# Performance work log

Measured on AMD Instinct MI355X. Metric: run time of the kernel, lower is better.

The kernel has to match this reference:

```python
import jax, jax.numpy as jnp
import numpy as np

N_FEATURES = 64
KERNEL = 3
PAD = KERNEL // 2


def setup_inputs() -> dict:
    key = jax.random.key(0)
    ks = jax.random.split(key, 6)
    B, C, D, H, W = 2, N_FEATURES, 64, 64, 64
    Q = jax.random.normal(ks[0], (B, C, D, H, W), dtype=jnp.float32)
    K = jax.random.normal(ks[1], (B, C, D, H, W), dtype=jnp.float32)
    V = jax.random.normal(ks[2], (B, C, D, H, W), dtype=jnp.float32)
    # learned params: positional embedding (torch.randn init) and 1x1x1 conv
    pos_emb = jax.random.normal(ks[3], (C, KERNEL, KERNEL, KERNEL), dtype=jnp.float32)
    fan_in = C  # 1x1x1 conv fan-in
    bound = 1.0 / np.sqrt(fan_in)
    W_out = jax.random.uniform(ks[4], (C, C), minval=-bound, maxval=bound, dtype=jnp.float32)
    b_out = jax.random.uniform(ks[5], (C,), minval=-bound, maxval=bound, dtype=jnp.float32)
    return {"Q": Q, "K": K, "V": V, "pos_emb": pos_emb, "W_out": W_out, "b_out": b_out}


def reference(Q, K, V, pos_emb, W_out, b_out):
    B, C, D, H, W = Q.shape
    scale = 1.0 / np.sqrt(C).astype(np.float32)
    pad = ((0, 0), (0, 0), (PAD, PAD), (PAD, PAD), (PAD, PAD))
    Kp = jnp.pad(K, pad)
    Vp = jnp.pad(V, pad)
    # scores over the 27 kernel offsets (fixed small loop; data dims vectorized)
    scores = []
    for i in range(KERNEL):
        for j in range(KERNEL):
            for k in range(KERNEL):
                Ks = Kp[:, :, i:i + D, j:j + H, k:k + W]  # (B,C,D,H,W)
                pe = pos_emb[:, i, j, k][None, :, None, None, None]
                scores.append(jnp.sum(Q * (Ks + pe), axis=1) * scale)  # (B,D,H,W)
    attn = jax.nn.softmax(jnp.stack(scores, axis=1), axis=1)  # (B,27,D,H,W)
    x = jnp.zeros_like(Q)
    ijk = 0
    for i in range(KERNEL):
        for j in range(KERNEL):
            for k in range(KERNEL):
                Vs = Vp[:, :, i:i + D, j:j + H, k:k + W]
                x = x + attn[:, ijk][:, None] * Vs
                ijk += 1
    # 1x1x1 conv projection
    out = jnp.einsum('oc,bcdhw->bodhw', W_out, x) + b_out[None, :, None, None, None]
    return out
```

## Files before the change

kernel.cpp:

```cpp
#include <hip/hip_runtime.h>
#include <math.h>

#define CH 64
#define S 64
#define S2 (64 * 64)
#define S3 (64 * 64 * 64)

__device__ float WT_buf[CH * CH];

__global__ __launch_bounds__(256) void wtrans(const float* __restrict__ W) {
  int i = blockIdx.x * 256 + threadIdx.x;
  int o = i >> 6, c = i & 63;
  WT_buf[c * CH + o] = W[o * CH + c];
}

__device__ __forceinline__ unsigned short f2bf(float f) {
  unsigned int u = __float_as_uint(f);
  return (unsigned short)((u + 0x7FFFu + ((u >> 16) & 1u)) >> 16);
}
__device__ __forceinline__ float bf2f(unsigned short s) {
  return __uint_as_float(((unsigned int)s) << 16);
}

__global__ __launch_bounds__(256) void attn_fused(const float* __restrict__ Q,
                                                  const float* __restrict__ K,
                                                  const float* __restrict__ V,
                                                  const float* __restrict__ pe,
                                                  const float* __restrict__ bias,
                                                  float* __restrict__ out) {
  __shared__ unsigned short xs[4][CH][64];
  int tid = threadIdx.x;
  int lane = tid & 63;
  int wv = tid >> 6;

  int raw = blockIdx.x;
  int sw = (raw & 7) * 256 + (raw >> 3);
  int b = sw >> 10;
  int r = sw & 1023;
  int d = r >> 4;
  int hu = __builtin_amdgcn_readfirstlane((r & 15) * 4 + wv);

  size_t bbase = (size_t)b << 24;
  const float* Qb = Q + bbase;
  const float* Kb = K + bbase;
  const float* Vb = V + bbase;
  float* outb = out + bbase;

  float lmL = (lane == 0) ? 0.f : 1.f;
  float lmR = (lane == 63) ? 0.f : 1.f;

  const float* krow[9];
  const float* vrow[9];
  float okf[9];
#pragma unroll
  for (int dz = 0; dz < 3; ++dz)
#pragma unroll
    for (int dy = 0; dy < 3; ++dy) {
      int rr = dz * 3 + dy;
      int zz = d + dz - 1, yy = hu + dy - 1;
      bool ok = ((unsigned)zz < 64u) & ((unsigned)yy < 64u);
      int zc = zz < 0 ? 0 : (zz > 63 ? 63 : zz);
      int yc = yy < 0 ? 0 : (yy > 63 ? 63 : yy);
      krow[rr] = Kb + zc * S2 + yc * S;
      vrow[rr] = Vb + zc * S2 + yc * S;
      okf[rr] = ok ? 1.f : 0.f;
    }
  int pos = d * S2 + hu * S + lane;

  float spe[27];
  float sC[9], sXR[9], sXL[9];
#pragma unroll
  for (int t = 0; t < 27; ++t) spe[t] = 0.f;
#pragma unroll
  for (int rr = 0; rr < 9; ++rr) { sC[rr] = 0.f; sXR[rr] = 0.f; sXL[rr] = 0.f; }

#pragma unroll 4
  for (int c = 0; c < CH; ++c) {
    int coff = c * S3;
    float q = Qb[coff + pos];
    float rv[9];
#pragma unroll
    for (int rr = 0; rr < 9; ++rr) rv[rr] = krow[rr][coff + lane];
    float qR = __shfl_down(q, 1);
    float qL = __shfl_up(q, 1);
#pragma unroll
    for (int rr = 0; rr < 9; ++rr) {
      sC[rr]  = fmaf(q,  rv[rr], sC[rr]);
      sXR[rr] = fmaf(qR, rv[rr], sXR[rr]);
      sXL[rr] = fmaf(qL, rv[rr], sXL[rr]);
    }
    const float* pec = pe + c * 27;
#pragma unroll
    for (int t = 0; t < 27; ++t) spe[t] = fmaf(q, pec[t], spe[t]);
  }

  float s[27];
#pragma unroll
  for (int rr = 0; rr < 9; ++rr) {
    float lt = __shfl_up(sXR[rr], 1);
    float rt = __shfl_down(sXL[rr], 1);
    s[rr * 3]     = fmaf(lt * lmL, okf[rr], spe[rr * 3]);
    s[rr * 3 + 1] = fmaf(sC[rr],   okf[rr], spe[rr * 3 + 1]);
    s[rr * 3 + 2] = fmaf(rt * lmR, okf[rr], spe[rr * 3 + 2]);
  }

  const float SC = 0.125f * 1.44269504088896f;
#pragma unroll
  for (int t = 0; t < 27; ++t) s[t] *= SC;
  float m = s[0];
#pragma unroll
  for (int t = 1; t < 27; ++t) m = fmaxf(m, s[t]);
  float sum = 0.f;
#pragma unroll
  for (int t = 0; t < 27; ++t) {
    s[t] = exp2f(s[t] - m);
    sum += s[t];
  }
  float inv = 1.f / sum;

  float wC[9], sLs[9], sRs[9];
#pragma unroll
  for (int rr = 0; rr < 9; ++rr) {
    float f = inv * okf[rr];
    float wL = s[rr * 3] * f;
    wC[rr]   = s[rr * 3 + 1] * f;
    float wR = s[rr * 3 + 2] * f;
    sLs[rr] = __shfl_down(wL, 1);
    sRs[rr] = __shfl_up(wR, 1);
  }

#pragma unroll 2
  for (int c = 0; c < CH; ++c) {
    int coff = c * S3;
    float rv[9];
#pragma unroll
    for (int rr = 0; rr < 9; ++rr) rv[rr] = vrow[rr][coff + lane];
    float own = 0.f, cR = 0.f, cL = 0.f;
#pragma unroll
    for (int rr = 0; rr < 9; ++rr) {
      own = fmaf(wC[rr], rv[rr], own);
      cR  = fmaf(sLs[rr], rv[rr], cR);
      cL  = fmaf(sRs[rr], rv[rr], cL);
    }
    float x_c = own + __shfl_up(cR, 1) * lmL + __shfl_down(cL, 1) * lmR;
    xs[wv][c][lane] = f2bf(x_c);
  }

#pragma unroll 1
  for (int ot = 0; ot < 4; ++ot) {
    float acc[16];
#pragma unroll
    for (int j = 0; j < 16; ++j) acc[j] = 0.f;
#pragma unroll 4
    for (int c = 0; c < CH; ++c) {
      float xc = bf2f(xs[wv][c][lane]);
      const float* wr = WT_buf + c * CH + ot * 16;
#pragma unroll
      for (int j = 0; j < 16; ++j) acc[j] = fmaf(wr[j], xc, acc[j]);
    }
#pragma unroll
    for (int j = 0; j < 16; ++j)
      outb[(ot * 16 + j) * S3 + pos] = acc[j] + bias[ot * 16 + j];
  }
}

extern "C" void kernel_launch(void* const* d_in, const int* in_sizes, int n_in,
                              void* d_out, int out_size, void* d_ws, size_t ws_size,
                              hipStream_t stream) {
  const float* Q = (const float*)d_in[0];
  const float* K = (const float*)d_in[1];
  const float* V = (const float*)d_in[2];
  const float* pe = (const float*)d_in[3];
  const float* W = (const float*)d_in[4];
  const float* bias = (const float*)d_in[5];
  float* out = (float*)d_out;

  wtrans<<<16, 256, 0, stream>>>(W);
  attn_fused<<<2048, 256, 0, stream>>>(Q, K, V, pe, bias, out);
}
```

Before: 234.7 us.

## Compute 1x1x1 output projection with bf16 MFMA instead of scalar FMAs

The 64x64 output projection now runs on the matrix cores via mfma_f32_16x16x32_bf16, with weights pre-converted to bf16 in a prep kernel and loaded as A fragments. The per-wave x tile in shared memory is transposed to [position][channel] with padding, and pairs of channels are packed per store so B fragments can be read as 8-element vectors. This removes a large scalar FMA loop and the scalar LDS reads, at the cost of bf16 weights (lower precision) and narrower output stores of 16 contiguous positions per row.

```diff
diff --git a/kernel.cpp b/kernel.cpp
--- a/kernel.cpp
+++ b/kernel.cpp
@@ -6,20 +6,19 @@
 #define S2 (64 * 64)
 #define S3 (64 * 64 * 64)
 
-__device__ float WT_buf[CH * CH];
-
-__global__ __launch_bounds__(256) void wtrans(const float* __restrict__ W) {
-  int i = blockIdx.x * 256 + threadIdx.x;
-  int o = i >> 6, c = i & 63;
-  WT_buf[c * CH + o] = W[o * CH + c];
-}
+typedef short short8_t __attribute__((ext_vector_type(8)));
+typedef float float4_t __attribute__((ext_vector_type(4)));
+
+__device__ __align__(16) unsigned short WB_buf[CH * CH];
 
 __device__ __forceinline__ unsigned short f2bf(float f) {
   unsigned int u = __float_as_uint(f);
   return (unsigned short)((u + 0x7FFFu + ((u >> 16) & 1u)) >> 16);
 }
-__device__ __forceinline__ float bf2f(unsigned short s) {
-  return __uint_as_float(((unsigned int)s) << 16);
+
+__global__ __launch_bounds__(256) void wprep(const float* __restrict__ W) {
+  int i = blockIdx.x * 256 + threadIdx.x;
+  WB_buf[i] = f2bf(W[i]);
 }
 
 __global__ __launch_bounds__(256) void attn_fused(const float* __restrict__ Q,
@@ -28,7 +27,7 @@
                                                   const float* __restrict__ pe,
                                                   const float* __restrict__ bias,
                                                   float* __restrict__ out) {
-  __shared__ unsigned short xs[4][CH][64];
+  __shared__ unsigned short xs[4][CH][68];
   int tid = threadIdx.x;
   int lane = tid & 63;
   int wv = tid >> 6;
@@ -65,7 +64,8 @@
       vrow[rr] = Vb + zc * S2 + yc * S;
       okf[rr] = ok ? 1.f : 0.f;
     }
-  int pos = d * S2 + hu * S + lane;
+  int upos = d * S2 + hu * S;
+  int pos = upos + lane;
 
   float spe[27];
   float sC[9], sXR[9], sXL[9];
@@ -130,37 +130,60 @@
   }
 
 #pragma unroll 2
-  for (int c = 0; c < CH; ++c) {
-    int coff = c * S3;
-    float rv[9];
-#pragma unroll
-    for (int rr = 0; rr < 9; ++rr) rv[rr] = vrow[rr][coff + lane];
-    float own = 0.f, cR = 0.f, cL = 0.f;
-#pragma unroll
-    for (int rr = 0; rr < 9; ++rr) {
-      own = fmaf(wC[rr], rv[rr], own);
-      cR  = fmaf(sLs[rr], rv[rr], cR);
-      cL  = fmaf(sRs[rr], rv[rr], cL);
-    }
-    float x_c = own + __shfl_up(cR, 1) * lmL + __shfl_down(cL, 1) * lmR;
-    xs[wv][c][lane] = f2bf(x_c);
-  }
+  for (int c2 = 0; c2 < CH; c2 += 2) {
+    unsigned int packed = 0;
+#pragma unroll
+    for (int u = 0; u < 2; ++u) {
+      int coff = (c2 + u) * S3;
+      float rv[9];
+#pragma unroll
+      for (int rr = 0; rr < 9; ++rr) rv[rr] = vrow[rr][coff + lane];
+      float own = 0.f, cR = 0.f, cL = 0.f;
+#pragma unroll
+      for (int rr = 0; rr < 9; ++rr) {
+        own = fmaf(wC[rr], rv[rr], own);
+        cR  = fmaf(sLs[rr], rv[rr], cR);
+        cL  = fmaf(sRs[rr], rv[rr], cL);
+      }
+      float x_c = own + __shfl_up(cR, 1) * lmL + __shfl_down(cL, 1) * lmR;
+      packed |= ((unsigned int)f2bf(x_c)) << (16 * u);
+    }
+    *(unsigned int*)&xs[wv][lane][c2] = packed;
+  }
+
+  __asm__ __volatile__("" ::: "memory");
+  __threadfence_block();
+
+  {
+    int n16 = lane & 15, g = lane >> 4;
+    short8_t afr[8];
+#pragma unroll
+    for (int ot = 0; ot < 4; ++ot)
+#pragma unroll
+      for (int kc = 0; kc < 2; ++kc)
+        afr[ot * 2 + kc] =
+            *(const short8_t*)(WB_buf + (ot * 16 + n16) * CH + kc * 32 + g * 8);
 
 #pragma unroll 1
-  for (int ot = 0; ot < 4; ++ot) {
-    float acc[16];
-#pragma unroll
-    for (int j = 0; j < 16; ++j) acc[j] = 0.f;
-#pragma unroll 4
-    for (int c = 0; c < CH; ++c) {
-      float xc = bf2f(xs[wv][c][lane]);
-      const float* wr = WT_buf + c * CH + ot * 16;
-#pragma unroll
-      for (int j = 0; j < 16; ++j) acc[j] = fmaf(wr[j], xc, acc[j]);
-    }
-#pragma unroll
-    for (int j = 0; j < 16; ++j)
-      outb[(ot * 16 + j) * S3 + pos] = acc[j] + bias[ot * 16 + j];
+    for (int pt = 0; pt < 4; ++pt) {
+      const unsigned short* bp = &xs[wv][pt * 16 + n16][g * 8];
+      union { short8_t v; uint2 h[2]; } u0, u1;
+      u0.h[0] = *(const uint2*)(bp);
+      u0.h[1] = *(const uint2*)(bp + 4);
+      u1.h[0] = *(const uint2*)(bp + 32);
+      u1.h[1] = *(const uint2*)(bp + 36);
+#pragma unroll
+      for (int ot = 0; ot < 4; ++ot) {
+        float4_t acc = {0.f, 0.f, 0.f, 0.f};
+        acc = __builtin_amdgcn_mfma_f32_16x16x32_bf16(afr[ot * 2],     u0.v, acc, 0, 0, 0);
+        acc = __builtin_amdgcn_mfma_f32_16x16x32_bf16(afr[ot * 2 + 1], u1.v, acc, 0, 0, 0);
+        int obase = ot * 16 + 4 * g;
+        float4_t bv = *(const float4_t*)(bias + obase);
+#pragma unroll
+        for (int j = 0; j < 4; ++j)
+          outb[(obase + j) * S3 + upos + pt * 16 + n16] = acc[j] + bv[j];
+      }
+    }
   }
 }
 
@@ -175,6 +198,6 @@
   const float* bias = (const float*)d_in[5];
   float* out = (float*)d_out;
 
-  wtrans<<<16, 256, 0, stream>>>(W);
+  wprep<<<16, 256, 0, stream>>>(W);
   attn_fused<<<2048, 256, 0, stream>>>(Q, K, V, pe, bias, out);
 }
```

Result: faster. 220.1 us (-6.2%).
